# Kernel optimization log

Hardware: AMD Instinct MI355X
Metric: run time of the kernel (lower is better)

The kernel has to match this reference:

```python
import jax, jax.numpy as jnp
import numpy as np

SIGMA1 = 0.02   # sigma1 init arg
K = 128         # number of discretization bins
TMIN = 1e-10
LEAKY_SLOPE = 0.01  # torch nn.LeakyReLU default


def setup_inputs() -> dict:
    key = jax.random.key(0)
    k1, k2, k3, k4, k5 = jax.random.split(key, 5)
    B, D, H = 256, 1024, 2048
    x = jax.random.uniform(k1, (B, D), jnp.float32, -1.0, 1.0)
    t = jax.random.uniform(k2, (B, 1), jnp.float32)          # Uniform(0,1) time sample
    noise = jax.random.normal(k3, (B, D), jnp.float32)       # for Normal sample of mu
    W1 = jax.random.normal(k4, (D + 1, H), jnp.float32) * (1.0 / np.sqrt(D + 1))
    b1 = jnp.zeros((H,), jnp.float32)
    W2 = jax.random.normal(k5, (H, 2 * D), jnp.float32) * (1.0 / np.sqrt(H))
    b2 = jnp.zeros((2 * D,), jnp.float32)
    return dict(x=x, t=t, noise=noise, W1=W1, b1=b1, W2=W2, b2=b2)


def _discretised_output_distribution(mu, t, gamma, W1, b1, W2, b2):
    B, D = mu.shape
    # NN: Linear -> LeakyReLU -> Linear, split into mu_eps / ln_sigma_eps
    h = jnp.concatenate([mu, t], axis=1) @ W1 + b1
    h = jnp.where(h >= 0, h, LEAKY_SLOPE * h)
    out = h @ W2 + b2
    mu_eps, ln_sig_eps = out[:, :D], out[:, D:]

    r = jnp.sqrt((1.0 - gamma) / gamma)                      # (B,1)
    mu_x = mu / gamma - r * mu_eps                           # (B,D)
    sigma_x = r * jnp.exp(ln_sig_eps)                        # (B,D)

    low_t = t < TMIN                                         # (B,1) rows with tiny t
    mu_x = jnp.where(low_t, 0.0, mu_x)
    sigma_x = jnp.where(low_t, 1.0, sigma_x)

    k = jnp.arange(K, dtype=jnp.float32)
    kl = 2.0 * (k - 1.0) / K - 1.0                           # left bin edge
    kr = 2.0 * k / K - 1.0                                   # right bin edge
    kc = (2.0 * k - 1.0) / K - 1.0                           # bin center weight

    inv = 1.0 / (sigma_x * jnp.sqrt(jnp.float32(2.0)))       # (B,D)

    def cdf(bound):  # bound: (K,) scalars -> clamped discretized CDF (B,D,K)
        F = 0.5 * (1.0 + jax.lax.erf((bound[None, None, :] - mu_x[:, :, None]) * inv[:, :, None]))
        return jnp.where(bound <= -1.0, 0.0, jnp.where(bound >= 1.0, 1.0, F))

    p = kc * (cdf(kr) - cdf(kl))                             # (B,D,K)
    return jnp.sum(p, axis=-1)                               # (B,D) expected value


def reference(x, t, noise, W1, b1, W2, b2):
    gamma = 1.0 - SIGMA1 ** (2.0 * t)                        # (B,1)
    # mu ~ Normal(gamma*x, std=gamma*(1-gamma)), reparameterized with noise
    mu = gamma * x + gamma * (1.0 - gamma) * noise
    pO = _discretised_output_distribution(mu, t, gamma, W1, b1, W2, b2)
    se = (x - pO) ** 2                                       # elementwise MSE
    loss = -jnp.log(jnp.float32(SIGMA1)) * jnp.mean(SIGMA1 ** (-2.0 * t) * se)
    return loss
```

## Files before the change

kernel.cpp:

```cpp
#include <hip/hip_runtime.h>
#include <hip/hip_bf16.h>
#include <math.h>


typedef __bf16 bf16_t;
typedef __bf16 bf16x8 __attribute__((ext_vector_type(8)));
typedef __bf16 bf16x4 __attribute__((ext_vector_type(4)));
typedef float  f32x4  __attribute__((ext_vector_type(4)));

#define LDK 40

__device__ __forceinline__ float erf_f(float x) {
  float ax = __builtin_fabsf(x);
  float t = __builtin_amdgcn_rcpf(fmaf(0.3275911f, ax, 1.0f));
  float p = fmaf(fmaf(fmaf(fmaf(1.061405429f, t, -1.453152027f), t, 1.421413741f),
                      t, -0.284496736f), t, 0.254829592f);
  p *= t;
  float e = __expf(-ax * ax);
  float r = fmaf(-p, e, 1.0f);
  return __builtin_copysignf(r, x);
}

__global__ __launch_bounds__(256, 2)
void prep_k(const float* __restrict__ x, const float* __restrict__ noise,
            const float* __restrict__ t, float4* __restrict__ rc4,
            bf16_t* __restrict__ A1) {
  int b = blockIdx.x;
  float tv = t[b];
  const float L2S = -5.6438561897747248f;
  float p = exp2f(2.0f * tv * L2S);
  float gamma = 1.0f - p;
  if (threadIdx.x == 0) {
    float r = sqrtf(p / gamma);
    float w = 1.0f / p;
    rc4[b] = make_float4(gamma, p, r, w);
  }
  int e = (b * 256 + threadIdx.x) * 4;
  float4 xv = *(const float4*)(x + e);
  float4 nv = *(const float4*)(noise + e);
  float g = gamma, gom = gamma * p;
  bf16x4 o;
  o[0] = (__bf16)(g * xv.x + gom * nv.x);
  o[1] = (__bf16)(g * xv.y + gom * nv.y);
  o[2] = (__bf16)(g * xv.z + gom * nv.z);
  o[3] = (__bf16)(g * xv.w + gom * nv.w);
  *(bf16x4*)(A1 + e) = o;
}

__global__ __launch_bounds__(256, 2)
void gemm_k(const bf16_t* __restrict__ A, int lda,
            const float* __restrict__ W, int N,
            float* __restrict__ P, int Ktiles, int Kchunk) {
  __shared__ bf16_t As[256 * LDK];
  __shared__ bf16_t Bs[32 * LDK];
  int tid = threadIdx.x;
  int lane = tid & 63, wave = tid >> 6;
  int n0 = blockIdx.x * 32;
  int k0 = blockIdx.z * Kchunk;
  int bn = tid & 31, bkg = tid >> 5;
  int fm = lane & 15, kq = lane >> 4;

  f32x4 acc[4][2];
#pragma unroll
  for (int i = 0; i < 4; ++i)
#pragma unroll
    for (int j = 0; j < 2; ++j) acc[i][j] = (f32x4)0.0f;

  for (int kt = 0; kt < Ktiles; ++kt) {
    int kb = k0 + kt * 32;
    const bf16_t* Ar = A + (size_t)tid * lda + kb;
#pragma unroll
    for (int j = 0; j < 4; ++j)
      *(bf16x8*)(&As[tid * LDK + j * 8]) = *(const bf16x8*)(Ar + j * 8);
    {
      const float* Wp = W + (size_t)(kb + bkg * 4) * N + n0 + bn;
      bf16x4 bv;
#pragma unroll
      for (int i = 0; i < 4; ++i) bv[i] = (__bf16)Wp[(size_t)i * N];
      *(bf16x4*)(&Bs[bn * LDK + bkg * 4]) = bv;
    }
    __syncthreads();
    bf16x8 aF[4], bF[2];
#pragma unroll
    for (int i = 0; i < 4; ++i)
      aF[i] = *(const bf16x8*)(&As[(wave * 64 + i * 16 + fm) * LDK + kq * 8]);
#pragma unroll
    for (int j = 0; j < 2; ++j)
      bF[j] = *(const bf16x8*)(&Bs[(j * 16 + fm) * LDK + kq * 8]);
#pragma unroll
    for (int i = 0; i < 4; ++i)
#pragma unroll
      for (int j = 0; j < 2; ++j)
        acc[i][j] = __builtin_amdgcn_mfma_f32_16x16x32_bf16(aF[i], bF[j], acc[i][j], 0, 0, 0);
    __syncthreads();
  }
  float* Pp = P + (size_t)blockIdx.z * 256 * N + n0;
#pragma unroll
  for (int i = 0; i < 4; ++i) {
    int mrow = wave * 64 + i * 16 + kq * 4;
#pragma unroll
    for (int j = 0; j < 2; ++j)
#pragma unroll
      for (int r = 0; r < 4; ++r)
        Pp[(size_t)(mrow + r) * N + j * 16 + fm] = acc[i][j][r];
  }
}

__global__ __launch_bounds__(256, 2)
void reduce1_k(const float* __restrict__ P1, const float* __restrict__ W1,
               const float* __restrict__ b1, const float* __restrict__ t,
               bf16_t* __restrict__ h) {
  int e = (blockIdx.x * 256 + threadIdx.x) * 4;
  int b = e >> 11, n = e & 2047;
  float4 s = *(const float4*)(P1 + e);
#pragma unroll
  for (int sp = 1; sp < 8; ++sp) {
    float4 v = *(const float4*)(P1 + (size_t)sp * 524288 + e);
    s.x += v.x; s.y += v.y; s.z += v.z; s.w += v.w;
  }
  float tv = t[b];
  float4 wl = *(const float4*)(W1 + 1024 * 2048 + n);
  float4 bb = *(const float4*)(b1 + n);
  s.x += tv * wl.x + bb.x;
  s.y += tv * wl.y + bb.y;
  s.z += tv * wl.z + bb.z;
  s.w += tv * wl.w + bb.w;
  bf16x4 o;
  o[0] = (__bf16)(s.x >= 0.f ? s.x : 0.01f * s.x);
  o[1] = (__bf16)(s.y >= 0.f ? s.y : 0.01f * s.y);
  o[2] = (__bf16)(s.z >= 0.f ? s.z : 0.01f * s.z);
  o[3] = (__bf16)(s.w >= 0.f ? s.w : 0.01f * s.w);
  *(bf16x4*)(h + e) = o;
}

__global__ __launch_bounds__(256, 4)
void loss_k(const float* __restrict__ x, const float* __restrict__ noise,
            const float* __restrict__ P2, const float* __restrict__ b2,
            const float4* __restrict__ rc4, const float* __restrict__ t,
            float* __restrict__ out) {
  int gid = blockIdx.x * 256 + threadIdx.x;
  int b = gid >> 10, d = gid & 1023;
  float4 rc = rc4[b];
  float tv = t[b];
  float om = rc.y, r = rc.z, w = rc.w;
  bool lowt = tv < 1e-10f;
  int base2 = b * 2048 + d;
  float me = b2[d], lg = b2[1024 + d];
#pragma unroll
  for (int sp = 0; sp < 8; ++sp) {
    me += P2[(size_t)sp * 524288 + base2];
    lg += P2[(size_t)sp * 524288 + base2 + 1024];
  }
  float xs = x[gid], ns = noise[gid];

  float mu_x = xs + om * ns - r * me;
  float sig = r * __expf(lg);
  if (lowt) { mu_x = 0.f; sig = 1.f; }
  float invs = 0.70710678118654752f / sig;
  float a = invs * 0.015625f;
  float c0 = (1.f + mu_x) * invs;
  float m64 = 64.f * (1.f + mu_x);
  float wdt = 316.78383797157331f * sig;
  float lo = m64 - wdt, hi = m64 + wdt;
  int klo = (lo < 1.f) ? 1 : ((lo > 126.f) ? 127 : (int)ceilf(lo));
  int khi = (hi < 1.f) ? 0 : ((hi > 126.f) ? 126 : (int)floorf(hi));
  float ss = (float)(126 - khi) - (float)(klo - 1);
  if (khi >= klo) {
    if (a <= 1.0f) {
      float za = fmaf(a, (float)klo - 0.5f, -c0);
      float zb = fmaf(a, (float)khi + 0.5f, -c0);
      const float ISP = 0.56418958354775628f;
      float ea = __expf(-za * za), eb = __expf(-zb * zb);
      float Ga = fmaf(za, erf_f(za), ISP * ea);
      float Gb = fmaf(zb, erf_f(zb), ISP * eb);
      float S = (Gb - Ga) * __builtin_amdgcn_rcpf(a)
              - a * 0.047015889f * (eb - ea);
      ss += S;
    } else {
      for (int k = klo; k <= khi; ++k) ss += erf_f(fmaf(a, (float)k, -c0));
    }
  }
  float z127 = fmaf(a, 127.f, -c0);
  float pO = fmaf(0.48828125f, 1.f + erf_f(z127),
                  fmaf(-0.0078125f, ss, -0.984375f));
  float df = xs - pO;
  float accv = w * df * df;
#pragma unroll
  for (int off = 32; off > 0; off >>= 1) accv += __shfl_down(accv, off, 64);
  __shared__ float red[4];
  if ((threadIdx.x & 63) == 0) red[threadIdx.x >> 6] = accv;
  __syncthreads();
  if (threadIdx.x == 0) {
    const float SCALE = 3.9120230054281461f / 262144.0f;
    atomicAdd(out, (red[0] + red[1] + red[2] + red[3]) * SCALE);
  }
}

extern "C" void kernel_launch(void* const* d_in, const int* in_sizes, int n_in,
                              void* d_out, int out_size, void* d_ws, size_t ws_size,
                              hipStream_t stream) {
  const float* x     = (const float*)d_in[0];
  const float* t     = (const float*)d_in[1];
  const float* noise = (const float*)d_in[2];
  const float* W1    = (const float*)d_in[3];
  const float* b1    = (const float*)d_in[4];
  const float* W2    = (const float*)d_in[5];
  const float* b2    = (const float*)d_in[6];
  float* out = (float*)d_out;

  char* ws = (char*)d_ws;
  float4* rc4 = (float4*)ws;
  bf16_t* A1  = (bf16_t*)(ws + 8192);
  bf16_t* h   = (bf16_t*)(ws + 8192 + 524288);
  float*  P1  = (float*)(ws + 8192 + 524288 + 1048576);
  float*  P2  = (float*)(ws + 8192 + 524288 + 1048576 + 16777216);

  hipMemsetAsync(d_out, 0, sizeof(float), stream);
  prep_k<<<256, 256, 0, stream>>>(x, noise, t, rc4, A1);
  gemm_k<<<dim3(64, 1, 8), 256, 0, stream>>>(A1, 1024, W1, 2048, P1, 4, 128);
  reduce1_k<<<512, 256, 0, stream>>>(P1, W1, b1, t, h);
  gemm_k<<<dim3(64, 1, 8), 256, 0, stream>>>(h, 2048, W2, 2048, P2, 8, 256);
  loss_k<<<1024, 256, 0, stream>>>(x, noise, P2, b2, rc4, t, out);
}
```

Measured before the change: 126.2 us.

## Fuse mu computation into first GEMM and drop prep kernel and memset

The prep kernel that wrote a bf16 copy of mu is removed. The first GEMM now reads x and noise in fp32 and computes gamma*x + gamma*(1-gamma)*noise while staging the A tile. The output memset moves into reduce1_k, and loss_k recomputes the per-row gamma constants itself. Two launches and the A1 round-trip go away. In exchange, each of the 64 column blocks rereads fp32 x and noise, twice the bytes of the old bf16 A1.

Result: slower. 147.4 us (+16.8%).

```diff
diff --git a/kernel.cpp b/kernel.cpp
--- a/kernel.cpp
+++ b/kernel.cpp
@@ -9,6 +9,7 @@
 typedef float  f32x4  __attribute__((ext_vector_type(4)));
 
 #define LDK 40
+#define L2S -5.6438561897747248f
 
 __device__ __forceinline__ float erf_f(float x) {
   float ax = __builtin_fabsf(x);
@@ -22,51 +23,104 @@
 }
 
 __global__ __launch_bounds__(256, 2)
-void prep_k(const float* __restrict__ x, const float* __restrict__ noise,
-            const float* __restrict__ t, float4* __restrict__ rc4,
-            bf16_t* __restrict__ A1) {
-  int b = blockIdx.x;
-  float tv = t[b];
-  const float L2S = -5.6438561897747248f;
-  float p = exp2f(2.0f * tv * L2S);
-  float gamma = 1.0f - p;
-  if (threadIdx.x == 0) {
-    float r = sqrtf(p / gamma);
-    float w = 1.0f / p;
-    rc4[b] = make_float4(gamma, p, r, w);
-  }
-  int e = (b * 256 + threadIdx.x) * 4;
-  float4 xv = *(const float4*)(x + e);
-  float4 nv = *(const float4*)(noise + e);
-  float g = gamma, gom = gamma * p;
-  bf16x4 o;
-  o[0] = (__bf16)(g * xv.x + gom * nv.x);
-  o[1] = (__bf16)(g * xv.y + gom * nv.y);
-  o[2] = (__bf16)(g * xv.z + gom * nv.z);
-  o[3] = (__bf16)(g * xv.w + gom * nv.w);
-  *(bf16x4*)(A1 + e) = o;
-}
-
-__global__ __launch_bounds__(256, 2)
-void gemm_k(const bf16_t* __restrict__ A, int lda,
-            const float* __restrict__ W, int N,
-            float* __restrict__ P, int Ktiles, int Kchunk) {
+void gemm1_k(const float* __restrict__ x, const float* __restrict__ noise,
+             const float* __restrict__ t, const float* __restrict__ W1,
+             float* __restrict__ P1) {
   __shared__ bf16_t As[256 * LDK];
   __shared__ bf16_t Bs[32 * LDK];
+  const int N = 2048;
   int tid = threadIdx.x;
   int lane = tid & 63, wave = tid >> 6;
   int n0 = blockIdx.x * 32;
-  int k0 = blockIdx.z * Kchunk;
+  int k0 = blockIdx.z * 128;
   int bn = tid & 31, bkg = tid >> 5;
   int fm = lane & 15, kq = lane >> 4;
 
+  float tv = t[tid];
+  float pr = exp2f(2.0f * tv * L2S);
+  float g = 1.0f - pr, gom = g * pr;
+
   f32x4 acc[4][2];
 #pragma unroll
   for (int i = 0; i < 4; ++i)
 #pragma unroll
     for (int j = 0; j < 2; ++j) acc[i][j] = (f32x4)0.0f;
 
-  for (int kt = 0; kt < Ktiles; ++kt) {
+  for (int kt = 0; kt < 4; ++kt) {
+    int kb = k0 + kt * 32;
+    const float* xr = x + (size_t)tid * 1024 + kb;
+    const float* nr = noise + (size_t)tid * 1024 + kb;
+#pragma unroll
+    for (int j = 0; j < 4; ++j) {
+      float4 xa = *(const float4*)(xr + j * 8);
+      float4 xb = *(const float4*)(xr + j * 8 + 4);
+      float4 na = *(const float4*)(nr + j * 8);
+      float4 nb = *(const float4*)(nr + j * 8 + 4);
+      bf16x8 o;
+      o[0] = (__bf16)fmaf(gom, na.x, g * xa.x);
+      o[1] = (__bf16)fmaf(gom, na.y, g * xa.y);
+      o[2] = (__bf16)fmaf(gom, na.z, g * xa.z);
+      o[3] = (__bf16)fmaf(gom, na.w, g * xa.w);
+      o[4] = (__bf16)fmaf(gom, nb.x, g * xb.x);
+      o[5] = (__bf16)fmaf(gom, nb.y, g * xb.y);
+      o[6] = (__bf16)fmaf(gom, nb.z, g * xb.z);
+      o[7] = (__bf16)fmaf(gom, nb.w, g * xb.w);
+      *(bf16x8*)(&As[tid * LDK + j * 8]) = o;
+    }
+    {
+      const float* Wp = W1 + (size_t)(kb + bkg * 4) * N + n0 + bn;
+      bf16x4 bv;
+#pragma unroll
+      for (int i = 0; i < 4; ++i) bv[i] = (__bf16)Wp[(size_t)i * N];
+      *(bf16x4*)(&Bs[bn * LDK + bkg * 4]) = bv;
+    }
+    __syncthreads();
+    bf16x8 aF[4], bF[2];
+#pragma unroll
+    for (int i = 0; i < 4; ++i)
+      aF[i] = *(const bf16x8*)(&As[(wave * 64 + i * 16 + fm) * LDK + kq * 8]);
+#pragma unroll
+    for (int j = 0; j < 2; ++j)
+      bF[j] = *(const bf16x8*)(&Bs[(j * 16 + fm) * LDK + kq * 8]);
+#pragma unroll
+    for (int i = 0; i < 4; ++i)
+#pragma unroll
+      for (int j = 0; j < 2; ++j)
+        acc[i][j] = __builtin_amdgcn_mfma_f32_16x16x32_bf16(aF[i], bF[j], acc[i][j], 0, 0, 0);
+    __syncthreads();
+  }
+  float* Pp = P1 + (size_t)blockIdx.z * 256 * N + n0;
+#pragma unroll
+  for (int i = 0; i < 4; ++i) {
+    int mrow = wave * 64 + i * 16 + kq * 4;
+#pragma unroll
+    for (int j = 0; j < 2; ++j)
+#pragma unroll
+      for (int r = 0; r < 4; ++r)
+        Pp[(size_t)(mrow + r) * N + j * 16 + fm] = acc[i][j][r];
+  }
+}
+
+__global__ __launch_bounds__(256, 2)
+void gemm2_k(const bf16_t* __restrict__ A, const float* __restrict__ W,
+             float* __restrict__ P) {
+  __shared__ bf16_t As[256 * LDK];
+  __shared__ bf16_t Bs[32 * LDK];
+  const int N = 2048, lda = 2048;
+  int tid = threadIdx.x;
+  int lane = tid & 63, wave = tid >> 6;
+  int n0 = blockIdx.x * 32;
+  int k0 = blockIdx.z * 256;
+  int bn = tid & 31, bkg = tid >> 5;
+  int fm = lane & 15, kq = lane >> 4;
+
+  f32x4 acc[4][2];
+#pragma unroll
+  for (int i = 0; i < 4; ++i)
+#pragma unroll
+    for (int j = 0; j < 2; ++j) acc[i][j] = (f32x4)0.0f;
+
+  for (int kt = 0; kt < 8; ++kt) {
     int kb = k0 + kt * 32;
     const bf16_t* Ar = A + (size_t)tid * lda + kb;
 #pragma unroll
@@ -109,7 +163,8 @@
 __global__ __launch_bounds__(256, 2)
 void reduce1_k(const float* __restrict__ P1, const float* __restrict__ W1,
                const float* __restrict__ b1, const float* __restrict__ t,
-               bf16_t* __restrict__ h) {
+               bf16_t* __restrict__ h, float* __restrict__ out) {
+  if (blockIdx.x == 0 && threadIdx.x == 0) *out = 0.0f;
   int e = (blockIdx.x * 256 + threadIdx.x) * 4;
   int b = e >> 11, n = e & 2047;
   float4 s = *(const float4*)(P1 + e);
@@ -136,13 +191,14 @@
 __global__ __launch_bounds__(256, 4)
 void loss_k(const float* __restrict__ x, const float* __restrict__ noise,
             const float* __restrict__ P2, const float* __restrict__ b2,
-            const float4* __restrict__ rc4, const float* __restrict__ t,
-            float* __restrict__ out) {
+            const float* __restrict__ t, float* __restrict__ out) {
   int gid = blockIdx.x * 256 + threadIdx.x;
   int b = gid >> 10, d = gid & 1023;
-  float4 rc = rc4[b];
   float tv = t[b];
-  float om = rc.y, r = rc.z, w = rc.w;
+  float om = exp2f(2.0f * tv * L2S);
+  float gamma = 1.0f - om;
+  float r = sqrtf(om / gamma);
+  float w = 1.0f / om;
   bool lowt = tv < 1e-10f;
   int base2 = b * 2048 + d;
   float me = b2[d], lg = b2[1024 + d];
@@ -209,16 +265,12 @@
   float* out = (float*)d_out;
 
   char* ws = (char*)d_ws;
-  float4* rc4 = (float4*)ws;
-  bf16_t* A1  = (bf16_t*)(ws + 8192);
-  bf16_t* h   = (bf16_t*)(ws + 8192 + 524288);
-  float*  P1  = (float*)(ws + 8192 + 524288 + 1048576);
-  float*  P2  = (float*)(ws + 8192 + 524288 + 1048576 + 16777216);
-
-  hipMemsetAsync(d_out, 0, sizeof(float), stream);
-  prep_k<<<256, 256, 0, stream>>>(x, noise, t, rc4, A1);
-  gemm_k<<<dim3(64, 1, 8), 256, 0, stream>>>(A1, 1024, W1, 2048, P1, 4, 128);
-  reduce1_k<<<512, 256, 0, stream>>>(P1, W1, b1, t, h);
-  gemm_k<<<dim3(64, 1, 8), 256, 0, stream>>>(h, 2048, W2, 2048, P2, 8, 256);
-  loss_k<<<1024, 256, 0, stream>>>(x, noise, P2, b2, rc4, t, out);
-}
+  bf16_t* h  = (bf16_t*)ws;
+  float*  P1 = (float*)(ws + 1048576);
+  float*  P2 = (float*)(ws + 1048576 + 16777216);
+
+  gemm1_k<<<dim3(64, 1, 8), 256, 0, stream>>>(x, noise, t, W1, P1);
+  reduce1_k<<<512, 256, 0, stream>>>(P1, W1, b1, t, h, out);
+  gemm2_k<<<dim3(64, 1, 8), 256, 0, stream>>>(h, W2, P2);
+  loss_k<<<1024, 256, 0, stream>>>(x, noise, P2, b2, t, out);
+}
```
